# Kernel tuning notes

Measured on AMD Instinct MI355X. Metric: run time of the kernel, lower is better.

## Reference

```python
import jax, jax.numpy as jnp
import numpy as np

INF = 1e20


def setup_inputs() -> dict:
    key = jax.random.key(0)
    k0, k1, k2, k3, k4 = jax.random.split(key, 5)
    B, T, C, D = 4, 8, 512, 256
    P, Ks = 4, 4
    return {
        "context": jax.random.normal(k0, (B, T, C, D), jnp.float32),
        "ctx_mask": jax.random.randint(k1, (B, C), 0, 2).astype(jnp.int32),
        "weight_tensor": jax.random.normal(k2, (P, D), jnp.float32),
        "mean_dis": jax.random.uniform(k3, (Ks, 1), jnp.float32),
        "precision_inv_dis": jax.random.uniform(k4, (Ks, 1), jnp.float32),
        "topk": 10,
        "max_position_distance": 160,
    }


def _forward(context, ctx_mask, weight_tensor, mean_dis, precision_inv_dis, topk, max_position_distance):
    B, T, C, D = context.shape
    Ks = mean_dis.shape[0]
    # attention[b,t,c,e] = mean_p sum_d ctx[b,t,c,d]*relu(W[p,d])*ctx[b,t,e,d]
    # (mean over perspectives commutes with the contraction over d)
    wbar = jnp.mean(jax.nn.relu(weight_tensor), axis=0)  # (D,)
    attention = jnp.einsum('btcd,bted->btce', context * wbar, context)  # (B,T,C,C)

    valid = ctx_mask > 0  # (B,C)
    pair_ok = valid[:, None, :, None] & valid[:, None, None, :]  # (B,1,C,C)
    attention = jnp.where(pair_ok, attention, -INF)

    # spatial Gaussian kernels over |i-j| distances (shared across batch/turn)
    idx = jnp.arange(C)
    pc = jnp.abs(idx[:, None] - idx[None, :]).astype(jnp.float32)
    pc = jnp.minimum(pc, float(max_position_distance)) / float(max_position_distance)  # (C,C)
    mu = mean_dis[:, 0][:, None, None]            # (Ks,1,1)
    prec = precision_inv_dis[:, 0][:, None, None]  # (Ks,1,1)
    spatial = jnp.exp(-0.5 * (pc[None] - mu) ** 2 * prec ** 2)  # (Ks,C,C)

    # kNN sparsification
    knn_val, knn_ind = jax.lax.top_k(attention, topk)  # (B,T,C,K)
    sem = jax.nn.softmax(knn_val, axis=-1)             # semantic weights (B,T,C,K)

    idx5 = jnp.broadcast_to(knn_ind[:, :, None, :, :], (B, T, Ks, C, topk))
    spatial_full = jnp.broadcast_to(spatial[None, None], (B, T, Ks, C, C))
    sp_chosen = jnp.take_along_axis(spatial_full, idx5, axis=-1)  # (B,T,Ks,C,K)
    sp_chosen = sp_chosen / jnp.sum(sp_chosen, axis=-1, keepdims=True)

    attn_chosen = sem[:, :, None, :, :] * sp_chosen  # (B,T,Ks,C,K)

    adj = jnp.zeros((B, T, Ks, C, C), dtype=attn_chosen.dtype)
    adj = adj.at[
        jnp.arange(B)[:, None, None, None, None],
        jnp.arange(T)[None, :, None, None, None],
        jnp.arange(Ks)[None, None, :, None, None],
        jnp.arange(C)[None, None, None, :, None],
        idx5,
    ].set(attn_chosen)
    return adj


def reference(context, ctx_mask, weight_tensor, mean_dis, precision_inv_dis, topk, max_position_distance):
    return _forward(context, ctx_mask, weight_tensor, mean_dis, precision_inv_dis, topk, max_position_distance)
```

## Files before the change

kernel.cpp:

```cpp
#include <hip/hip_runtime.h>
#include <math.h>

#define C_ 512
#define D_ 256
#define KS_ 4
#define TOPK_ 10
#define NEG 1e20f

typedef float v2f __attribute__((ext_vector_type(2)));
typedef float v4f __attribute__((ext_vector_type(4)));

__device__ __forceinline__ int csw2(int g) { return g ^ ((g >> 3) & 1); }

#define ASTR 36
#define ASTR3 68
#define BSTR2 260
#define ABUF3 (16 * ASTR3)
#define BBUF3 (16 * BSTR2)

#define PKFMA_LO(ACC, AP, BP) \
    asm("v_pk_fma_f32 %0, %1, %2, %0 op_sel:[0,0,0] op_sel_hi:[0,1,1]" \
        : "+v"(ACC) : "v"(AP), "v"(BP));
#define PKFMA_HI(ACC, AP, BP) \
    asm("v_pk_fma_f32 %0, %1, %2, %0 op_sel:[1,0,0] op_sel_hi:[1,1,1]" \
        : "+v"(ACC) : "v"(AP), "v"(BP));

extern "C" __global__ __launch_bounds__(256, 2)
void gemm_attn(const float* __restrict__ ctx,
               const float* __restrict__ W,
               float* __restrict__ ws)
{
    __shared__ __align__(16) float wbar_s[D_];
    __shared__ __align__(16) float a_s[2 * ABUF3];
    __shared__ __align__(16) float b_s[2 * BBUF3];

    const int tid  = threadIdx.x;
    const int lane = tid & 63;
    const int wv   = tid >> 6;
    const int wr   = (wv >> 1) * 32;
    const int wc   = (wv & 1) * 128;
    const int rg   = lane >> 4;
    const int cg   = lane & 15;

    const int blk  = blockIdx.x;
    const int bt   = (blk & 7) * 4 + ((blk >> 3) & 3);
    const int tile = blk >> 5;
    const int c0   = (tile & 7) * 64;
    const int n0   = (tile >> 3) * 256;

    const float* ctx_bt = ctx + (size_t)bt * (C_ * D_);

    {
        float w0 = W[tid], w1 = W[D_ + tid], w2 = W[2 * D_ + tid], w3 = W[3 * D_ + tid];
        wbar_s[tid] = 0.25f * (fmaxf(w0, 0.f) + fmaxf(w1, 0.f) + fmaxf(w2, 0.f) + fmaxf(w3, 0.f));
    }

    const int bcol = tid >> 2;
    const int bq   = tid & 3;
    const float* bsrc = ctx_bt + (size_t)(n0 + bcol) * D_ + bq * 4;
    const int bwoff = (4 * bq) * BSTR2 + bcol;
    const int ar_ = tid >> 2;
    const int aq  = tid & 3;
    const float* asrc = ctx_bt + (size_t)(c0 + ar_) * D_ + aq * 4;
    const int awoff = (4 * aq) * ASTR3 + ar_;
    const int abase = wr + rg * 8;
    const int bbase = wc + cg * 4;

    __syncthreads();

    {
        v4f B0 = *(const v4f*)(bsrc + (size_t)0 * 64 * D_);
        v4f B1 = *(const v4f*)(bsrc + (size_t)1 * 64 * D_);
        v4f B2 = *(const v4f*)(bsrc + (size_t)2 * 64 * D_);
        v4f B3 = *(const v4f*)(bsrc + (size_t)3 * 64 * D_);
        v4f A0 = *(const v4f*)asrc;
        #pragma unroll
        for (int j = 0; j < 4; ++j) {
            b_s[bwoff + j * BSTR2 + 0 * 64] = B0[j];
            b_s[bwoff + j * BSTR2 + 1 * 64] = B1[j];
            b_s[bwoff + j * BSTR2 + 2 * 64] = B2[j];
            b_s[bwoff + j * BSTR2 + 3 * 64] = B3[j];
        }
        v4f wb = *(const v4f*)(wbar_s + aq * 4);
        a_s[awoff + 0 * ASTR3] = A0[0] * wb[0];
        a_s[awoff + 1 * ASTR3] = A0[1] * wb[1];
        a_s[awoff + 2 * ASTR3] = A0[2] * wb[2];
        a_s[awoff + 3 * ASTR3] = A0[3] * wb[3];
    }
    __syncthreads();

    v2f acc2[8][4];
    #pragma unroll
    for (int j = 0; j < 8; ++j)
        #pragma unroll
        for (int t = 0; t < 4; ++t) acc2[j][t] = (v2f){0.f, 0.f};

    #define FMA_RANGE(K0, K1)                                                 \
        _Pragma("unroll")                                                     \
        for (int kk = (K0); kk < (K1); ++kk) {                                \
            v4f av0 = *(const v4f*)(acur + kk * ASTR3 + abase);               \
            v4f av1 = *(const v4f*)(acur + kk * ASTR3 + abase + 4);           \
            v4f bv0 = *(const v4f*)(bcur + kk * BSTR2 + bbase);               \
            v4f bv1 = *(const v4f*)(bcur + kk * BSTR2 + bbase + 64);          \
            v2f a01 = __builtin_shufflevector(av0, av0, 0, 1);                \
            v2f a23 = __builtin_shufflevector(av0, av0, 2, 3);                \
            v2f a45 = __builtin_shufflevector(av1, av1, 0, 1);                \
            v2f a67 = __builtin_shufflevector(av1, av1, 2, 3);                \
            v2f b0l = __builtin_shufflevector(bv0, bv0, 0, 1);                \
            v2f b0h = __builtin_shufflevector(bv0, bv0, 2, 3);                \
            v2f b1l = __builtin_shufflevector(bv1, bv1, 0, 1);                \
            v2f b1h = __builtin_shufflevector(bv1, bv1, 2, 3);                \
            PKFMA_LO(acc2[0][0], a01, b0l) PKFMA_LO(acc2[0][1], a01, b0h)     \
            PKFMA_LO(acc2[0][2], a01, b1l) PKFMA_LO(acc2[0][3], a01, b1h)     \
            PKFMA_HI(acc2[1][0], a01, b0l) PKFMA_HI(acc2[1][1], a01, b0h)     \
            PKFMA_HI(acc2[1][2], a01, b1l) PKFMA_HI(acc2[1][3], a01, b1h)     \
            PKFMA_LO(acc2[2][0], a23, b0l) PKFMA_LO(acc2[2][1], a23, b0h)     \
            PKFMA_LO(acc2[2][2], a23, b1l) PKFMA_LO(acc2[2][3], a23, b1h)     \
            PKFMA_HI(acc2[3][0], a23, b0l) PKFMA_HI(acc2[3][1], a23, b0h)     \
            PKFMA_HI(acc2[3][2], a23, b1l) PKFMA_HI(acc2[3][3], a23, b1h)     \
            PKFMA_LO(acc2[4][0], a45, b0l) PKFMA_LO(acc2[4][1], a45, b0h)     \
            PKFMA_LO(acc2[4][2], a45, b1l) PKFMA_LO(acc2[4][3], a45, b1h)     \
            PKFMA_HI(acc2[5][0], a45, b0l) PKFMA_HI(acc2[5][1], a45, b0h)     \
            PKFMA_HI(acc2[5][2], a45, b1l) PKFMA_HI(acc2[5][3], a45, b1h)     \
            PKFMA_LO(acc2[6][0], a67, b0l) PKFMA_LO(acc2[6][1], a67, b0h)     \
            PKFMA_LO(acc2[6][2], a67, b1l) PKFMA_LO(acc2[6][3], a67, b1h)     \
            PKFMA_HI(acc2[7][0], a67, b0l) PKFMA_HI(acc2[7][1], a67, b0h)     \
            PKFMA_HI(acc2[7][2], a67, b1l) PKFMA_HI(acc2[7][3], a67, b1h)     \
        }

    for (int kt = 0; kt < 16; ++kt) {
        const float* acur = a_s + (kt & 1) * ABUF3;
        const float* bcur = b_s + (kt & 1) * BBUF3;
        float* anx = a_s + ((kt & 1) ^ 1) * ABUF3;
        float* bnx = b_s + ((kt & 1) ^ 1) * BBUF3;
        const bool pf = (kt < 15);

        v4f B0, B1, B2, B3, A0;
        if (pf) {
            const float* nb = bsrc + (kt + 1) * 16;
            B0 = *(const v4f*)(nb + (size_t)0 * 64 * D_);
            B1 = *(const v4f*)(nb + (size_t)1 * 64 * D_);
            B2 = *(const v4f*)(nb + (size_t)2 * 64 * D_);
            B3 = *(const v4f*)(nb + (size_t)3 * 64 * D_);
            A0 = *(const v4f*)(asrc + (kt + 1) * 16);
        }
        FMA_RANGE(0, 10)
        if (pf) {
            #pragma unroll
            for (int j = 0; j < 4; ++j) {
                bnx[bwoff + j * BSTR2 + 0 * 64] = B0[j];
                bnx[bwoff + j * BSTR2 + 1 * 64] = B1[j];
                bnx[bwoff + j * BSTR2 + 2 * 64] = B2[j];
                bnx[bwoff + j * BSTR2 + 3 * 64] = B3[j];
            }
            v4f wb = *(const v4f*)(wbar_s + (kt + 1) * 16 + aq * 4);
            anx[awoff + 0 * ASTR3] = A0[0] * wb[0];
            anx[awoff + 1 * ASTR3] = A0[1] * wb[1];
            anx[awoff + 2 * ASTR3] = A0[2] * wb[2];
            anx[awoff + 3 * ASTR3] = A0[3] * wb[3];
        }
        FMA_RANGE(10, 16)
        __syncthreads();
    }
    #undef FMA_RANGE

    #pragma unroll
    for (int j = 0; j < 8; ++j) {
        float* wrow = ws + ((size_t)bt * C_ + c0 + wr + rg * 8 + j) * C_ + n0;
        v4f o0 = __builtin_shufflevector(acc2[j][0], acc2[j][1], 0, 1, 2, 3);
        v4f o1 = __builtin_shufflevector(acc2[j][2], acc2[j][3], 0, 1, 2, 3);
        *(v4f*)(wrow + bbase)      = o0;
        *(v4f*)(wrow + bbase + 64) = o1;
    }
}

extern "C" __global__ __launch_bounds__(256, 2)
void epilogue_k(const float* __restrict__ ws,
                const int* __restrict__ cmask,
                const float* __restrict__ mu_g,
                const float* __restrict__ pr_g,
                float* __restrict__ out)
{
    const int tid  = threadIdx.x;
    const int lane = tid & 63;
    const int wv   = tid >> 6;

    const int blk = blockIdx.x;
    const int bt  = blk >> 7;
    const int rq  = blk & 127;
    const int b   = bt >> 3;

    {
        const float4 z = make_float4(0.f, 0.f, 0.f, 0.f);
        #pragma unroll
        for (int ks = 0; ks < KS_; ++ks) {
            float* ob = out + ((size_t)(bt * KS_ + ks) * C_ + rq * 4) * C_;
            *(float4*)(ob + (size_t)tid * 4)         = z;
            *(float4*)(ob + (size_t)(tid + 256) * 4) = z;
        }
    }

    const int c  = rq * 4 + wv;
    const int vr = cmask[b * C_ + c];

    float row[8];
    {
        const float* wrow = ws + ((size_t)bt * C_ + c) * C_ + lane * 8;
        float4 r0 = *(const float4*)wrow;
        float4 r1 = *(const float4*)(wrow + 4);
        row[0] = r0.x; row[1] = r0.y; row[2] = r0.z; row[3] = r0.w;
        row[4] = r1.x; row[5] = r1.y; row[6] = r1.z; row[7] = r1.w;
        int4 m0 = *(const int4*)(cmask + b * C_ + lane * 8);
        int4 m1 = *(const int4*)(cmask + b * C_ + lane * 8 + 4);
        int em[8] = {m0.x, m0.y, m0.z, m0.w, m1.x, m1.y, m1.z, m1.w};
        #pragma unroll
        for (int i = 0; i < 8; ++i) {
            bool ok = (vr > 0) && (em[i] > 0);
            row[i] = ok ? row[i] : -NEG;
        }
    }

    float tv[TOPK_];
    int   te[TOPK_];
    unsigned int taken = 0;
    #pragma unroll
    for (int j = 0; j < TOPK_; ++j) {
        float lv = -3.3e38f;
        int   li = 0;
        #pragma unroll
        for (int i = 0; i < 8; ++i) {
            bool better = (!((taken >> i) & 1u)) && (row[i] > lv);
            lv = better ? row[i] : lv;
            li = better ? i : li;
        }
        int le = lane * 8 + li;
        #pragma unroll
        for (int off = 1; off < 64; off <<= 1) {
            float ov = __shfl_xor(lv, off);
            int   oe = __shfl_xor(le, off);
            bool take = (ov > lv) || (ov == lv && oe < le);
            lv = take ? ov : lv;
            le = take ? oe : le;
        }
        tv[j] = lv;
        te[j] = le;
        if ((le >> 3) == lane) taken |= 1u << (le & 7);
    }
    const float mx = tv[0];
    float ssum = 0.f;
    #pragma unroll
    for (int j = 0; j < TOPK_; ++j) ssum += expf(tv[j] - mx);

    float oval = 0.f;
    size_t ooff = 0;
    {
        const int ksq = (lane < 40) ? (lane / 10) : 3;
        const int myj = (lane < 40) ? (lane - (lane / 10) * 10) : 0;
        const float mu = mu_g[ksq];
        const float pr = pr_g[ksq];
        float sps = 0.f, spj = 0.f, tvj = 0.f;
        int ej = 0;
        #pragma unroll
        for (int j = 0; j < TOPK_; ++j) {
            float d = fabsf((float)(te[j] - c));
            d = fminf(d, 160.f) * (1.0f / 160.0f);
            float x  = d - mu;
            float sp = expf(-0.5f * x * x * pr * pr);
            sps += sp;
            if (j == myj) { spj = sp; tvj = tv[j]; ej = te[j]; }
        }
        oval = (expf(tvj - mx) / ssum) * (spj / sps);
        ooff = ((size_t)(bt * KS_ + ksq) * C_ + c) * C_ + ej;
    }

    __syncthreads();
    if (lane < 40) out[ooff] = oval;
}

#define BSTR 516
extern "C" __global__ __launch_bounds__(256, 2)
void graph_learner(const float* __restrict__ ctx,
                   const int* __restrict__ cmask,
                   const float* __restrict__ W,
                   const float* __restrict__ mu_g,
                   const float* __restrict__ pr_g,
                   float* __restrict__ out)
{
    __shared__ __align__(16) float wbar_s[D_];
    __shared__ __align__(16) float a_s[16 * ASTR];
    __shared__ __align__(16) float b_s[16 * BSTR];
    __shared__ __align__(8)  float res_s[2560];
    __shared__ unsigned int vmask_s[16];

    const int tid  = threadIdx.x;
    const int lane = tid & 63;
    const int wv   = tid >> 6;
    const int w8   = wv * 8;

    const int blk = blockIdx.x;
    const int bt  = (blk & 7) * 4 + ((blk >> 3) & 3);
    const int c0  = (blk >> 5) * 32;
    const int b   = bt >> 3;

    const float* ctx_bt = ctx + (size_t)bt * (C_ * D_);
    const int*   mask_b = cmask + b * C_;

    {
        float w0 = W[tid], w1 = W[D_ + tid], w2 = W[2 * D_ + tid], w3 = W[3 * D_ + tid];
        wbar_s[tid] = 0.25f * (fmaxf(w0, 0.f) + fmaxf(w1, 0.f) + fmaxf(w2, 0.f) + fmaxf(w3, 0.f));
    }
    if (tid < 16) {
        unsigned int m = 0;
        for (int i = 0; i < 32; ++i)
            m |= (mask_b[tid * 32 + i] > 0 ? 1u : 0u) << i;
        vmask_s[tid] = m;
    }

    const int brow = tid >> 2;
    const int bq   = tid & 3;
    const float* bsrc = ctx_bt + (size_t)brow * D_ + bq * 4;
    const int bwbase = (4 * bq) * BSTR + 4 * csw2(brow >> 2) + (brow & 3);
    const int ar_ = tid >> 2;
    const int aq  = tid & 3;
    const float* asrc = ctx_bt + (size_t)(c0 + ar_) * D_ + aq * 4;
    const int awbase = (4 * aq) * ASTR + ar_;
    const int bc0 = 4 * csw2(2 * lane);
    const int bc1 = 4 * csw2(2 * lane + 1);

    v2f acc2[8][4];
    #pragma unroll
    for (int j = 0; j < 8; ++j)
        #pragma unroll
        for (int t = 0; t < 4; ++t) acc2[j][t] = (v2f){0.f, 0.f};

    for (int kt = 0; kt < 16; ++kt) {
        __syncthreads();
        #pragma unroll
        for (int i = 0; i < 8; ++i) {
            float4 v = *(const float4*)(bsrc + (size_t)i * 64 * D_ + kt * 16);
            b_s[bwbase + 0 * BSTR + i * 64] = v.x;
            b_s[bwbase + 1 * BSTR + i * 64] = v.y;
            b_s[bwbase + 2 * BSTR + i * 64] = v.z;
            b_s[bwbase + 3 * BSTR + i * 64] = v.w;
        }
        if (tid < 128) {
            float4 v  = *(const float4*)(asrc + kt * 16);
            float4 wb = *(const float4*)(wbar_s + kt * 16 + aq * 4);
            a_s[awbase + 0 * ASTR] = v.x * wb.x;
            a_s[awbase + 1 * ASTR] = v.y * wb.y;
            a_s[awbase + 2 * ASTR] = v.z * wb.z;
            a_s[awbase + 3 * ASTR] = v.w * wb.w;
        }
        __syncthreads();
        #pragma unroll
        for (int kk = 0; kk < 16; ++kk) {
            float4 av0 = *(const float4*)(a_s + kk * ASTR + w8);
            float4 av1 = *(const float4*)(a_s + kk * ASTR + w8 + 4);
            float4 bv0 = *(const float4*)(b_s + kk * BSTR + bc0);
            float4 bv1 = *(const float4*)(b_s + kk * BSTR + bc1);
            v2f b20 = (v2f){bv0.x, bv0.y};
            v2f b21 = (v2f){bv0.z, bv0.w};
            v2f b22 = (v2f){bv1.x, bv1.y};
            v2f b23 = (v2f){bv1.z, bv1.w};
            float ar8[8] = {av0.x, av0.y, av0.z, av0.w, av1.x, av1.y, av1.z, av1.w};
            #pragma unroll
            for (int j = 0; j < 8; ++j) {
                v2f a2 = (v2f){ar8[j], ar8[j]};
                asm("v_pk_fma_f32 %0, %1, %2, %0" : "+v"(acc2[j][0]) : "v"(a2), "v"(b20));
                asm("v_pk_fma_f32 %0, %1, %2, %0" : "+v"(acc2[j][1]) : "v"(a2), "v"(b21));
                asm("v_pk_fma_f32 %0, %1, %2, %0" : "+v"(acc2[j][2]) : "v"(a2), "v"(b22));
                asm("v_pk_fma_f32 %0, %1, %2, %0" : "+v"(acc2[j][3]) : "v"(a2), "v"(b23));
            }
        }
    }

    {
        const float4 z = make_float4(0.f, 0.f, 0.f, 0.f);
        #pragma unroll
        for (int ks = 0; ks < KS_; ++ks) {
            float* ob = out + ((size_t)(bt * KS_ + ks) * C_ + c0) * C_;
            #pragma unroll
            for (int i = 0; i < 16; ++i)
                *(float4*)(ob + (size_t)(tid + i * 256) * 4) = z;
        }
    }

    const unsigned int em8 = (vmask_s[lane >> 2] >> ((lane & 3) * 8)) & 0xffu;
    const float mu0 = mu_g[0], mu1 = mu_g[1], mu2 = mu_g[2], mu3 = mu_g[3];
    const float pr0 = pr_g[0], pr1 = pr_g[1], pr2 = pr_g[2], pr3 = pr_g[3];

    #pragma unroll
    for (int jr = 0; jr < 8; ++jr) {
        const int c  = c0 + w8 + jr;
        const int vr = mask_b[c];
        float row[8];
        #pragma unroll
        for (int t = 0; t < 4; ++t) { row[2 * t] = acc2[jr][t].x; row[2 * t + 1] = acc2[jr][t].y; }
        #pragma unroll
        for (int i = 0; i < 8; ++i) {
            bool ok = (vr > 0) && ((em8 >> i) & 1u);
            row[i] = ok ? row[i] : -NEG;
        }
        float tv[TOPK_];
        int   te[TOPK_];
        unsigned int taken = 0;
        #pragma unroll
        for (int j = 0; j < TOPK_; ++j) {
            float lv = -3.3e38f;
            int   li = 0;
            #pragma unroll
            for (int i = 0; i < 8; ++i) {
                bool better = (!((taken >> i) & 1u)) && (row[i] > lv);
                lv = better ? row[i] : lv;
                li = better ? i : li;
            }
            int le = lane * 8 + li;
            #pragma unroll
            for (int off = 1; off < 64; off <<= 1) {
                float ov = __shfl_xor(lv, off);
                int   oe = __shfl_xor(le, off);
                bool take = (ov > lv) || (ov == lv && oe < le);
                lv = take ? ov : lv;
                le = take ? oe : le;
            }
            tv[j] = lv;
            te[j] = le;
            if ((le >> 3) == lane) taken |= 1u << (le & 7);
        }
        const float mx = tv[0];
        float ssum = 0.f;
        #pragma unroll
        for (int j = 0; j < TOPK_; ++j) ssum += expf(tv[j] - mx);

        if (lane < 40) {
            const int ksq = lane / 10;
            const int myj = lane - ksq * 10;
            const float mu = (ksq == 0) ? mu0 : (ksq == 1) ? mu1 : (ksq == 2) ? mu2 : mu3;
            const float pr = (ksq == 0) ? pr0 : (ksq == 1) ? pr1 : (ksq == 2) ? pr2 : pr3;
            float sps = 0.f, spj = 0.f, tvj = 0.f;
            int ej = 0;
            #pragma unroll
            for (int j = 0; j < TOPK_; ++j) {
                float d = fabsf((float)(te[j] - c));
                d = fminf(d, 160.f) * (1.0f / 160.0f);
                float x  = d - mu;
                float sp = expf(-0.5f * x * x * pr * pr);
                sps += sp;
                if (j == myj) { spj = sp; tvj = tv[j]; ej = te[j]; }
            }
            float val = (expf(tvj - mx) / ssum) * (spj / sps);
            int   off = ((bt * KS_ + ksq) * C_ + c) * C_ + ej;
            int   slot = (((wv * 8 + jr) * 40) + lane) * 2;
            res_s[slot]     = val;
            res_s[slot + 1] = __int_as_float(off);
        }
    }

    __syncthreads();
    #pragma unroll
    for (int i = 0; i < 5; ++i) {
        int p = tid * 5 + i;
        float v   = res_s[2 * p];
        int   off = __float_as_int(res_s[2 * p + 1]);
        out[off] = v;
    }
}

extern "C" void kernel_launch(void* const* d_in, const int* in_sizes, int n_in,
                              void* d_out, int out_size, void* d_ws, size_t ws_size,
                              hipStream_t stream) {
    (void)in_sizes; (void)n_in; (void)out_size;
    const float* ctx   = (const float*)d_in[0];
    const int*   cmask = (const int*)d_in[1];
    const float* W     = (const float*)d_in[2];
    const float* mu    = (const float*)d_in[3];
    const float* pr    = (const float*)d_in[4];
    const size_t WS_NEEDED = (size_t)32 * C_ * C_ * sizeof(float);
    if (ws_size >= WS_NEEDED) {
        float* ws = (float*)d_ws;
        gemm_attn<<<dim3(512), dim3(256), 0, stream>>>(ctx, W, ws);
        epilogue_k<<<dim3(4096), dim3(256), 0, stream>>>(ws, cmask, mu, pr, (float*)d_out);
    } else {
        graph_learner<<<dim3(512), dim3(256), 0, stream>>>(ctx, cmask, W, mu, pr, (float*)d_out);
    }
}
```

Measured before the change: 95.00 us.

## Move output zero-fill into GEMM main loop to overlap with compute

The zeroing of the large output tensor moves out of the epilogue kernel and into the GEMM kernel's K loop. Each of the 512 blocks writes 64K floats spread over the 16 iterations, so those stores can overlap with the FMA work. The epilogue then drops its __syncthreads and scatters its top-k values directly. Correctness relies on the kernels running in order on the same stream. The extra store traffic may compete with the GEMM's global loads.

```diff
diff --git a/kernel.cpp b/kernel.cpp
--- a/kernel.cpp
+++ b/kernel.cpp
@@ -28,7 +28,8 @@
 extern "C" __global__ __launch_bounds__(256, 2)
 void gemm_attn(const float* __restrict__ ctx,
                const float* __restrict__ W,
-               float* __restrict__ ws)
+               float* __restrict__ ws,
+               float* __restrict__ out)
 {
     __shared__ __align__(16) float wbar_s[D_];
     __shared__ __align__(16) float a_s[2 * ABUF3];
@@ -49,6 +50,7 @@
     const int n0   = (tile >> 3) * 256;
 
     const float* ctx_bt = ctx + (size_t)bt * (C_ * D_);
+    float* zbase = out + (size_t)blk * 65536 + (size_t)tid * 4;
 
     {
         float w0 = W[tid], w1 = W[D_ + tid], w2 = W[2 * D_ + tid], w3 = W[3 * D_ + tid];
@@ -128,6 +130,8 @@
             PKFMA_HI(acc2[7][2], a67, b1l) PKFMA_HI(acc2[7][3], a67, b1h)     \
         }
 
+    const v4f zv = (v4f){0.f, 0.f, 0.f, 0.f};
+
     for (int kt = 0; kt < 16; ++kt) {
         const float* acur = a_s + (kt & 1) * ABUF3;
         const float* bcur = b_s + (kt & 1) * BBUF3;
@@ -144,6 +148,10 @@
             B3 = *(const v4f*)(nb + (size_t)3 * 64 * D_);
             A0 = *(const v4f*)(asrc + (kt + 1) * 16);
         }
+        #pragma unroll
+        for (int q = 0; q < 4; ++q)
+            *(v4f*)(zbase + (size_t)(kt * 4 + q) * 1024) = zv;
+
         FMA_RANGE(0, 10)
         if (pf) {
             #pragma unroll
@@ -190,16 +198,6 @@
     const int rq  = blk & 127;
     const int b   = bt >> 3;
 
-    {
-        const float4 z = make_float4(0.f, 0.f, 0.f, 0.f);
-        #pragma unroll
-        for (int ks = 0; ks < KS_; ++ks) {
-            float* ob = out + ((size_t)(bt * KS_ + ks) * C_ + rq * 4) * C_;
-            *(float4*)(ob + (size_t)tid * 4)         = z;
-            *(float4*)(ob + (size_t)(tid + 256) * 4) = z;
-        }
-    }
-
     const int c  = rq * 4 + wv;
     const int vr = cmask[b * C_ + c];
 
@@ -251,11 +249,9 @@
     #pragma unroll
     for (int j = 0; j < TOPK_; ++j) ssum += expf(tv[j] - mx);
 
-    float oval = 0.f;
-    size_t ooff = 0;
-    {
-        const int ksq = (lane < 40) ? (lane / 10) : 3;
-        const int myj = (lane < 40) ? (lane - (lane / 10) * 10) : 0;
+    if (lane < 40) {
+        const int ksq = lane / 10;
+        const int myj = lane - ksq * 10;
         const float mu = mu_g[ksq];
         const float pr = pr_g[ksq];
         float sps = 0.f, spj = 0.f, tvj = 0.f;
@@ -269,12 +265,9 @@
             sps += sp;
             if (j == myj) { spj = sp; tvj = tv[j]; ej = te[j]; }
         }
-        oval = (expf(tvj - mx) / ssum) * (spj / sps);
-        ooff = ((size_t)(bt * KS_ + ksq) * C_ + c) * C_ + ej;
-    }
-
-    __syncthreads();
-    if (lane < 40) out[ooff] = oval;
+        float oval = (expf(tvj - mx) / ssum) * (spj / sps);
+        out[((size_t)(bt * KS_ + ksq) * C_ + c) * C_ + ej] = oval;
+    }
 }
 
 #define BSTR 516
@@ -478,7 +471,7 @@
     const size_t WS_NEEDED = (size_t)32 * C_ * C_ * sizeof(float);
     if (ws_size >= WS_NEEDED) {
         float* ws = (float*)d_ws;
-        gemm_attn<<<dim3(512), dim3(256), 0, stream>>>(ctx, W, ws);
+        gemm_attn<<<dim3(512), dim3(256), 0, stream>>>(ctx, W, ws, (float*)d_out);
         epilogue_k<<<dim3(4096), dim3(256), 0, stream>>>(ws, cmask, mu, pr, (float*)d_out);
     } else {
         graph_learner<<<dim3(512), dim3(256), 0, stream>>>(ctx, cmask, W, mu, pr, (float*)d_out);
```

Result: no change. 94.47 us (-0.6%).
